# Performance work log

Hardware: AMD Instinct MI355X
Metric: run time of the kernel (lower is better)

The kernel has to match this reference:

```python
import jax, jax.numpy as jnp
import numpy as np

N, D, H, E, K = 16384, 1024, 4096, 8, 2
EPS = 1e-5


def setup_inputs() -> dict:
    key = jax.random.key(0)
    ks = jax.random.split(key, 12)
    s = 0.02
    return {
        "x": jax.random.normal(ks[0], (N, D), dtype=jnp.float32),
        "ln_g": jnp.ones((D,), jnp.float32),
        "ln_b": jnp.zeros((D,), jnp.float32),
        "r_w1": jax.random.normal(ks[1], (D, H // 2), jnp.float32) * s,
        "r_b1": jnp.zeros((H // 2,), jnp.float32),
        "r_w2": jax.random.normal(ks[2], (H // 2, E), jnp.float32) * s,
        "r_b2": jnp.zeros((E,), jnp.float32),
        "e_w1": jax.random.normal(ks[3], (E, D, H), jnp.float32) * s,
        "e_b1": jnp.zeros((E, H), jnp.float32),
        "e_w2": jax.random.normal(ks[4], (E, H, D), jnp.float32) * s,
        "e_b2": jnp.zeros((E, D), jnp.float32),
    }


def reference(x, ln_g, ln_b, r_w1, r_b1, r_w2, r_b2, e_w1, e_b1, e_w2, e_b2):
    # LayerNorm
    mu = jnp.mean(x, axis=-1, keepdims=True)
    var = jnp.mean(jnp.square(x - mu), axis=-1, keepdims=True)
    xn = (x - mu) * jax.lax.rsqrt(var + EPS) * ln_g + ln_b  # [N, D]

    # Router: Linear -> ReLU -> Linear -> softmax -> top-k, renormalize
    logits = jax.nn.relu(xn @ r_w1 + r_b1) @ r_w2 + r_b2  # [N, E]
    probs = jax.nn.softmax(logits, axis=-1)
    vals, idx = jax.lax.top_k(probs, K)  # [N, K]
    vals = vals / jnp.sum(vals, axis=-1, keepdims=True)

    # Dense expert dispatch: loop over fixed small E, weight by combine gate
    out = jnp.zeros_like(x)
    for e in range(E):
        gate = jnp.sum(vals * (idx == e).astype(vals.dtype), axis=-1)  # [N]
        h = jax.nn.relu(xn @ e_w1[e] + e_b1[e])  # dropout in eval mode -> identity
        y = h @ e_w2[e] + e_b2[e]  # [N, D]
        out = out + gate[:, None] * y
    return x + out
```

## Files before the change

kernel.cpp:

```cpp
#include <hip/hip_runtime.h>
#include <cstdint>
#include <cstddef>

typedef unsigned short u16;
typedef __attribute__((ext_vector_type(8))) short bf16x8;
typedef __attribute__((ext_vector_type(4))) float f32x4;

#define N_TOK 16384
#define DIM   1024
#define HID   4096
#define NEXP  8
#define HR    2048
#define TAU   0.02f
#define MAXMT 264

__device__ __forceinline__ u16 f2bf(float f) {
  union { float f; uint32_t u; } x; x.f = f;
  uint32_t r = x.u + 0x7FFFu + ((x.u >> 16) & 1u);
  return (u16)(r >> 16);
}
__device__ __forceinline__ float bf2f(u16 u) {
  union { uint32_t u; float f; } x; x.u = ((uint32_t)u) << 16; return x.f;
}

__device__ __forceinline__ void async16(const void* g, const void* l) {
  auto gp = reinterpret_cast<const __attribute__((address_space(1))) uint32_t*>(
      reinterpret_cast<uintptr_t>(g));
  auto lp = reinterpret_cast<__attribute__((address_space(3))) uint32_t*>(
      reinterpret_cast<uintptr_t>(l));
  __builtin_amdgcn_global_load_lds(gp, lp, 16, 0, 0);
}

__device__ __forceinline__ unsigned xcd_swz(unsigned flat, unsigned nwg) {
  const unsigned xcd = flat & 7u, lid = flat >> 3;
  const unsigned q = nwg >> 3, r = nwg & 7u;
  return (xcd < r ? xcd * (q + 1u) : r * (q + 1u) + (xcd - r) * q) + lid;
}

template<bool SPLIT>
__global__ __launch_bounds__(256)
void transpose_cvt(const float* __restrict__ src, u16* __restrict__ hi,
                   u16* __restrict__ lo, int R, int C)
{
  __shared__ float tile[32][33];
  const size_t bofs = (size_t)blockIdx.z * R * C;
  src += bofs; hi += bofs; if (SPLIT) lo += bofs;
  const int tx = threadIdx.x, ty = threadIdx.y;
  const int c0 = blockIdx.x * 32, r0 = blockIdx.y * 32;
#pragma unroll
  for (int i = 0; i < 4; ++i)
    tile[ty + i * 8][tx] = src[(size_t)(r0 + ty + i * 8) * C + c0 + tx];
  __syncthreads();
#pragma unroll
  for (int i = 0; i < 4; ++i) {
    float v = tile[tx][ty + i * 8];
    size_t o = (size_t)(c0 + ty + i * 8) * R + r0 + tx;
    u16 h = f2bf(v);
    hi[o] = h;
    if (SPLIT) lo[o] = f2bf(v - bf2f(h));
  }
}

__global__ __launch_bounds__(256)
void ln_kernel(const float* __restrict__ x, const float* __restrict__ g,
               const float* __restrict__ b, u16* __restrict__ xh,
               u16* __restrict__ xl, float* __restrict__ out)
{
  const int row = blockIdx.x;
  const int t = threadIdx.x;
  const float4 xv = ((const float4*)(x + (size_t)row * DIM))[t];
  float s = xv.x + xv.y + xv.z + xv.w;
  float q = xv.x * xv.x + xv.y * xv.y + xv.z * xv.z + xv.w * xv.w;
#pragma unroll
  for (int off = 32; off; off >>= 1) {
    s += __shfl_down(s, off, 64);
    q += __shfl_down(q, off, 64);
  }
  __shared__ float sm[8];
  __shared__ float mu_s, rs_s;
  const int lane = t & 63, wv = t >> 6;
  if (lane == 0) { sm[wv] = s; sm[wv + 4] = q; }
  __syncthreads();
  if (t == 0) {
    float S = sm[0] + sm[1] + sm[2] + sm[3];
    float Q = sm[4] + sm[5] + sm[6] + sm[7];
    float mu = S * (1.f / DIM);
    float var = Q * (1.f / DIM) - mu * mu;
    mu_s = mu; rs_s = rsqrtf(var + 1e-5f);
  }
  __syncthreads();
  const float mu = mu_s, rs = rs_s;
  const float4 gv = ((const float4*)g)[t];
  const float4 bv = ((const float4*)b)[t];
  float n0 = (xv.x - mu) * rs * gv.x + bv.x;
  float n1 = (xv.y - mu) * rs * gv.y + bv.y;
  float n2 = (xv.z - mu) * rs * gv.z + bv.z;
  float n3 = (xv.w - mu) * rs * gv.w + bv.w;
  ushort4 h, l;
  h.x = f2bf(n0); l.x = f2bf(n0 - bf2f(h.x));
  h.y = f2bf(n1); l.y = f2bf(n1 - bf2f(h.y));
  h.z = f2bf(n2); l.z = f2bf(n2 - bf2f(h.z));
  h.w = f2bf(n3); l.w = f2bf(n3 - bf2f(h.w));
  ((ushort4*)(xh + (size_t)row * DIM))[t] = h;
  ((ushort4*)(xl + (size_t)row * DIM))[t] = l;
  ((float4*)(out + (size_t)row * DIM))[t] = xv;
}

__global__ __launch_bounds__(256)
void logits_kernel(const u16* __restrict__ HrB, const float* __restrict__ w2,
                   float* __restrict__ logits)
{
  const int row = blockIdx.x, t = threadIdx.x;
  const u16* h = HrB + (size_t)row * HR;
  const ushort4* hv = (const ushort4*)(h + t * 8);
  ushort4 h0 = hv[0], h1 = hv[1];
  u16 hh[8] = {h0.x, h0.y, h0.z, h0.w, h1.x, h1.y, h1.z, h1.w};
  float p[8] = {0, 0, 0, 0, 0, 0, 0, 0};
#pragma unroll
  for (int j = 0; j < 8; ++j) {
    const int col = t * 8 + j;
    const float v = bf2f(hh[j]);
    const float4* wp = (const float4*)(w2 + (size_t)col * 8);
    float4 a = wp[0], b = wp[1];
    p[0] += v * a.x; p[1] += v * a.y; p[2] += v * a.z; p[3] += v * a.w;
    p[4] += v * b.x; p[5] += v * b.y; p[6] += v * b.z; p[7] += v * b.w;
  }
#pragma unroll
  for (int off = 32; off; off >>= 1)
#pragma unroll
    for (int e = 0; e < 8; ++e) p[e] += __shfl_down(p[e], off, 64);
  __shared__ float sm[4][8];
  const int lane = t & 63, wv = t >> 6;
  if (lane == 0) {
#pragma unroll
    for (int e = 0; e < 8; ++e) sm[wv][e] = p[e];
  }
  __syncthreads();
  if (t < 8)
    logits[(size_t)row * 8 + t] = sm[0][t] + sm[1][t] + sm[2][t] + sm[3][t];
}

__device__ __forceinline__ void load_logits(const float* logits, const float* b2,
                                            int row, float l[8]) {
  const float4* lp = (const float4*)(logits + (size_t)row * 8);
  float4 a = lp[0], b = lp[1];
  l[0] = a.x + b2[0]; l[1] = a.y + b2[1]; l[2] = a.z + b2[2]; l[3] = a.w + b2[3];
  l[4] = b.x + b2[4]; l[5] = b.y + b2[5]; l[6] = b.z + b2[6]; l[7] = b.w + b2[7];
}
__device__ __forceinline__ void top2(const float l[8], int& i0, float& l0,
                                     int& i1, float& l1) {
  i0 = 0; l0 = l[0];
#pragma unroll
  for (int e = 1; e < 8; ++e) if (l[e] > l0) { l0 = l[e]; i0 = e; }
  i1 = -1; l1 = -1e30f;
#pragma unroll
  for (int e = 0; e < 8; ++e) if (e != i0 && l[e] > l1) { l1 = l[e]; i1 = e; }
}

__global__ __launch_bounds__(256)
void pass_flag(float* __restrict__ logits, const float* __restrict__ b2,
               int* __restrict__ fixL, int* __restrict__ cntFix)
{
  __shared__ int lcnt;
  __shared__ int base;
  const int t = threadIdx.x;
  const int row = blockIdx.x * 256 + t;
  if (t == 0) lcnt = 0;
  float l[8]; load_logits(logits, b2, row, l);
  int i0, i1; float l0, l1;
  top2(l, i0, l0, i1, l1);
  float l2 = -1e30f;
#pragma unroll
  for (int e = 0; e < 8; ++e)
    if (e != i0 && e != i1 && l[e] > l2) l2 = l[e];
  const bool flag = (l1 - l2) < TAU;
  __syncthreads();
  int r = 0;
  if (flag) r = atomicAdd(&lcnt, 1);
  __syncthreads();
  if (t == 0) base = atomicAdd(cntFix, lcnt);
  __syncthreads();
  if (flag) {
    fixL[base + r] = row;
    float4 z = {0.f, 0.f, 0.f, 0.f};
    ((float4*)(logits + (size_t)row * 8))[0] = z;
    ((float4*)(logits + (size_t)row * 8))[1] = z;
  }
}

__global__ __launch_bounds__(256)
void pass_count(const float* __restrict__ logits, const float* __restrict__ b2,
                int* __restrict__ cnts)
{
  __shared__ int lcnt[NEXP];
  const int t = threadIdx.x;
  const int row = blockIdx.x * 256 + t;
  if (t < NEXP) lcnt[t] = 0;
  float l[8]; load_logits(logits, b2, row, l);
  int i0, i1; float l0, l1;
  top2(l, i0, l0, i1, l1);
  __syncthreads();
  atomicAdd(&lcnt[i0], 1);
  atomicAdd(&lcnt[i1], 1);
  __syncthreads();
  if (t < NEXP) atomicAdd(&cnts[t], lcnt[t]);
}

__global__ void scan_kernel(const int* __restrict__ cnts, int* __restrict__ offs,
                            int* __restrict__ tileOffs)
{
  if (threadIdx.x == 0) {
    int s = 0, ts = 0;
#pragma unroll
    for (int e = 0; e < NEXP; ++e) {
      offs[e] = s; s += cnts[e];
      tileOffs[e] = ts; ts += (cnts[e] + 127) >> 7;
    }
    offs[NEXP] = s;
    tileOffs[NEXP] = ts;
  }
}

__global__ __launch_bounds__(256)
void pass_scatter(const float* __restrict__ logits, const float* __restrict__ b2,
                  const int* __restrict__ offs, int* __restrict__ cnts2,
                  int* __restrict__ rowsC, float* __restrict__ gateC)
{
  __shared__ int lcnt[NEXP];
  __shared__ int sbase[NEXP];
  const int t = threadIdx.x;
  const int row = blockIdx.x * 256 + t;
  if (t < NEXP) lcnt[t] = 0;
  float l[8]; load_logits(logits, b2, row, l);
  int i0, i1; float l0, l1;
  top2(l, i0, l0, i1, l1);
  float tt = expf(l1 - l0);
  float g0 = 1.f / (1.f + tt);
  float g1 = tt / (1.f + tt);
  __syncthreads();
  int r0 = atomicAdd(&lcnt[i0], 1);
  int r1 = atomicAdd(&lcnt[i1], 1);
  __syncthreads();
  if (t < NEXP) sbase[t] = atomicAdd(&cnts2[t], lcnt[t]);
  __syncthreads();
  int p0 = offs[i0] + sbase[i0] + r0;
  int p1 = offs[i1] + sbase[i1] + r1;
  rowsC[p0] = row; gateC[p0] = g0;
  rowsC[p1] = row; gateC[p1] = g1;
}

template<int EPI, bool GATHER>
__global__ __launch_bounds__(512, 2)
void gemm_moe(const u16* __restrict__ A0, const u16* __restrict__ B0,
              int lda, int ldb, int K, int NT,
              size_t bStrideE, int biasStrideE,
              const int* __restrict__ counts,
              const int* __restrict__ offs, const int* __restrict__ tileOffs,
              const int* __restrict__ rowsC, const float* __restrict__ gatesC,
              const float* __restrict__ bias,
              u16* __restrict__ Cbf, float* __restrict__ Cf32, int ldc)
{
  const unsigned swz = xcd_swz(blockIdx.x, gridDim.x);
  const int mt = (int)(swz / (unsigned)NT);
  if (mt >= tileOffs[NEXP]) return;
  int e = 0;
#pragma unroll
  for (int i = 1; i < NEXP; ++i) if (tileOffs[i] <= mt) e = i;
  const int m0 = (mt - tileOffs[e]) * 128;
  const int n0 = (int)(swz % (unsigned)NT) * 256;
  const int Mq = counts[e];
  if (m0 >= Mq) return;

  const int off = offs[e];
  const int* rows = rowsC + off;
  const u16* B = B0 + (size_t)e * bStrideE;
  const float* bi = bias + (size_t)e * biasStrideE;

  __shared__ alignas(16) u16 As[8][128 * 32];
  __shared__ alignas(16) u16 Bs[4][256 * 32];

  const int t = threadIdx.x;
  const int numK = K >> 5;

  const int rloc = t >> 2;
  const int cb = ((t & 3) << 4) ^ (((t >> 5) & 1) << 5);
  const int csrc = cb >> 1;
  const int arow0 = m0 + rloc;
  const int amc = arow0 < Mq ? arow0 : (Mq - 1);
  const size_t agr = GATHER ? (size_t)rows[amc] : (size_t)(off + amc);
  const u16* aSrc = A0 + agr * lda + csrc;
  const u16* bSrc0 = B + (size_t)(n0 + rloc) * ldb + csrc;
  const u16* bSrc1 = B + (size_t)(n0 + 128 + rloc) * ldb + csrc;

#pragma unroll
  for (int h = 0; h < 6; ++h)
    async16(aSrc + h * 32, &As[h][t * 8]);
#pragma unroll
  for (int h = 0; h < 3; ++h) {
    async16(bSrc0 + h * 32, &Bs[h][t * 8]);
    async16(bSrc1 + h * 32, &Bs[h][4096 + t * 8]);
  }
  asm volatile("s_waitcnt vmcnt(4)" ::: "memory");
  __builtin_amdgcn_s_barrier();
  __builtin_amdgcn_sched_barrier(0);

  const int lane = t & 63, wv = t >> 6;
  const int wm = wv >> 2;
  const int wn = wv & 3;
  const int fr = lane & 15, fq = lane >> 4;

  int aIdx[4], bIdx[4];
#pragma unroll
  for (int mf = 0; mf < 4; ++mf) {
    const int r = wm * 64 + mf * 16 + fr;
    aIdx[mf] = r * 32 + ((fq * 8) ^ (((r >> 3) & 1) << 4));
  }
#pragma unroll
  for (int nf = 0; nf < 4; ++nf) {
    const int rb = wn * 64 + nf * 16 + fr;
    bIdx[nf] = rb * 32 + ((fq * 8) ^ (((rb >> 3) & 1) << 4));
  }

  f32x4 acc[4][4];
#pragma unroll
  for (int i = 0; i < 4; ++i)
#pragma unroll
    for (int j = 0; j < 4; ++j) acc[i][j] = (f32x4){0.f, 0.f, 0.f, 0.f};

  for (int T = 0; T < numK; ++T) {
    const u16* aLds = As[T & 7];
    const u16* bLds = Bs[T & 3];
    bf16x8 aF[4], bF[4];
#pragma unroll
    for (int i = 0; i < 4; ++i) {
      aF[i] = *(const bf16x8*)&aLds[aIdx[i]];
      bF[i] = *(const bf16x8*)&bLds[bIdx[i]];
    }
    if (T + 3 < numK) {
      async16(bSrc0 + (T + 3) * 32, &Bs[(T + 3) & 3][t * 8]);
      async16(bSrc1 + (T + 3) * 32, &Bs[(T + 3) & 3][4096 + t * 8]);
    }
    if (T + 6 < numK) async16(aSrc + (T + 6) * 32, &As[(T + 6) & 7][t * 8]);

    __builtin_amdgcn_s_setprio(1);
#pragma unroll
    for (int mf = 0; mf < 4; ++mf)
#pragma unroll
      for (int nf = 0; nf < 4; ++nf)
        acc[mf][nf] = __builtin_amdgcn_mfma_f32_16x16x32_bf16(
            aF[mf], bF[nf], acc[mf][nf], 0, 0, 0);
    __builtin_amdgcn_s_setprio(0);
    __builtin_amdgcn_sched_barrier(0);

    const int rem = numK - T;
    if (T == 0)        { asm volatile("s_waitcnt vmcnt(5)" ::: "memory"); }
    else if (T == 1)   { asm volatile("s_waitcnt vmcnt(6)" ::: "memory"); }
    else if (rem >= 7) { asm volatile("s_waitcnt vmcnt(7)" ::: "memory"); }
    else if (rem == 6) { asm volatile("s_waitcnt vmcnt(6)" ::: "memory"); }
    else if (rem == 5) { asm volatile("s_waitcnt vmcnt(5)" ::: "memory"); }
    else if (rem == 4) { asm volatile("s_waitcnt vmcnt(4)" ::: "memory"); }
    else if (rem == 3) { asm volatile("s_waitcnt vmcnt(2)" ::: "memory"); }
    else               { asm volatile("s_waitcnt vmcnt(0)" ::: "memory"); }
    __builtin_amdgcn_s_barrier();
    __builtin_amdgcn_sched_barrier(0);
  }

  float bv[4];
#pragma unroll
  for (int nf = 0; nf < 4; ++nf) bv[nf] = bi[n0 + wn * 64 + nf * 16 + fr];

#pragma unroll
  for (int mf = 0; mf < 4; ++mf)
#pragma unroll
    for (int r = 0; r < 4; ++r) {
      const int m = m0 + wm * 64 + mf * 16 + fq * 4 + r;
      if (m < Mq) {
        if constexpr (EPI == 2) {
          const size_t orow = (size_t)rows[m];
          const float g = gatesC[off + m];
#pragma unroll
          for (int nf = 0; nf < 4; ++nf) {
            const int n = n0 + wn * 64 + nf * 16 + fr;
            atomicAdd(&Cf32[orow * ldc + n], g * (acc[mf][nf][r] + bv[nf]));
          }
        } else {
#pragma unroll
          for (int nf = 0; nf < 4; ++nf) {
            const int n = n0 + wn * 64 + nf * 16 + fr;
            Cbf[(size_t)(off + m) * ldc + n] =
                f2bf(fmaxf(acc[mf][nf][r] + bv[nf], 0.f));
          }
        }
      }
    }
}

template<bool SPLIT, int EPI, bool GATHER>
__global__ __launch_bounds__(256, 2)
void gemm_bt(const u16* __restrict__ A0, const u16* __restrict__ A1,
             const u16* __restrict__ B0, const u16* __restrict__ B1,
             int lda, int ldb, int K, int M,
             const int* __restrict__ counts, int expertArg,
             const int* __restrict__ offs,
             const int* __restrict__ rowsC, const float* __restrict__ gatesC,
             const float* __restrict__ bias,
             const float* __restrict__ w2, float* __restrict__ logits,
             u16* __restrict__ Cbf, float* __restrict__ Cf32, int ldc)
{
  int expert, m0, n0;
  if (counts == nullptr) {
    const unsigned nwg = gridDim.x * gridDim.y;
    const unsigned flat = blockIdx.y * gridDim.x + blockIdx.x;
    const unsigned swz = xcd_swz(flat, nwg);
    expert = expertArg;
    m0 = (int)(swz / gridDim.x) * 128;
    n0 = (int)(swz % gridDim.x) * 128;
  } else {
    expert = expertArg;
    m0 = blockIdx.y * 128;
    n0 = blockIdx.x * 128;
  }

  const int Mq = counts ? counts[expert] : M;
  if (m0 >= Mq) return;
  const int off = offs ? offs[expert] : 0;
  const int* rows = rowsC ? rowsC + off : nullptr;
  const float* gates = gatesC ? gatesC + off : nullptr;
  const u16* B = B0;
  const u16* Bl = SPLIT ? B1 : nullptr;
  const float* bi = bias;
  const int z = (int)blockIdx.z;
  const int zOff = z * K;

  __shared__ u16 As0[128 * 32], Bs0[128 * 32];
  __shared__ u16 As1[SPLIT ? 128 * 32 : 8], Bs1[SPLIT ? 128 * 32 : 8];

  const int t = threadIdx.x;
  size_t aoff[2]; int acodd[2]; size_t boff[2];
#pragma unroll
  for (int i = 0; i < 2; ++i) {
    int gdx = i * 256 + t;
    int ar = gdx >> 2, ac = (gdx & 3) * 8;
    int am = m0 + ar;
    int amc = am < Mq ? am : (Mq - 1);
    int agr = GATHER ? rows[amc] : amc;
    aoff[i] = (size_t)agr * lda + ac + zOff;
    boff[i] = (size_t)(n0 + ar) * ldb + ac + zOff;
    acodd[i] = gdx * 8;
  }

  f32x4 acc[4][4];
#pragma unroll
  for (int i = 0; i < 4; ++i)
#pragma unroll
    for (int j = 0; j < 4; ++j) acc[i][j] = (f32x4){0.f, 0.f, 0.f, 0.f};

  const int lane = t & 63, wv = t >> 6;
  const int wm = (wv >> 1) * 64, wn = (wv & 1) * 64;
  const int fr = lane & 15, fq = lane >> 4;

  for (int k0 = 0; k0 < K; k0 += 32) {
    __syncthreads();
#pragma unroll
    for (int i = 0; i < 2; ++i) {
      async16(A0 + aoff[i] + k0, &As0[acodd[i]]);
      async16(B + boff[i] + k0, &Bs0[acodd[i]]);
      if (SPLIT) {
        async16(A1 + aoff[i] + k0, &As1[acodd[i]]);
        async16(Bl + boff[i] + k0, &Bs1[acodd[i]]);
      }
    }
    __syncthreads();
    bf16x8 af[4], bfr[4], af1[4], bf1[4];
#pragma unroll
    for (int xi = 0; xi < 4; ++xi) {
      af[xi]  = *(const bf16x8*)&As0[(wm + xi * 16 + fr) * 32 + fq * 8];
      bfr[xi] = *(const bf16x8*)&Bs0[(wn + xi * 16 + fr) * 32 + fq * 8];
      if (SPLIT) {
        af1[xi] = *(const bf16x8*)&As1[(wm + xi * 16 + fr) * 32 + fq * 8];
        bf1[xi] = *(const bf16x8*)&Bs1[(wn + xi * 16 + fr) * 32 + fq * 8];
      }
    }
#pragma unroll
    for (int mt = 0; mt < 4; ++mt)
#pragma unroll
      for (int nt = 0; nt < 4; ++nt) {
        acc[mt][nt] = __builtin_amdgcn_mfma_f32_16x16x32_bf16(af[mt], bfr[nt], acc[mt][nt], 0, 0, 0);
        if (SPLIT) {
          acc[mt][nt] = __builtin_amdgcn_mfma_f32_16x16x32_bf16(af[mt], bf1[nt], acc[mt][nt], 0, 0, 0);
          acc[mt][nt] = __builtin_amdgcn_mfma_f32_16x16x32_bf16(af1[mt], bfr[nt], acc[mt][nt], 0, 0, 0);
        }
      }
  }

  if constexpr (EPI == 3) {
    float w2v[4][8]; float b1v[4];
#pragma unroll
    for (int nt = 0; nt < 4; ++nt) {
      const int n = n0 + wn + nt * 16 + fr;
      b1v[nt] = bi[n];
      const float4* wp = (const float4*)(w2 + (size_t)n * 8);
      float4 wa = wp[0], wb = wp[1];
      w2v[nt][0] = wa.x; w2v[nt][1] = wa.y; w2v[nt][2] = wa.z; w2v[nt][3] = wa.w;
      w2v[nt][4] = wb.x; w2v[nt][5] = wb.y; w2v[nt][6] = wb.z; w2v[nt][7] = wb.w;
    }
#pragma unroll
    for (int mt = 0; mt < 4; ++mt) {
      float pe[4][8];
#pragma unroll
      for (int r = 0; r < 4; ++r)
#pragma unroll
        for (int ee = 0; ee < 8; ++ee) pe[r][ee] = 0.f;
#pragma unroll
      for (int nt = 0; nt < 4; ++nt)
#pragma unroll
        for (int r = 0; r < 4; ++r) {
          float v = fmaxf(acc[mt][nt][r] + b1v[nt], 0.f);
#pragma unroll
          for (int ee = 0; ee < 8; ++ee) pe[r][ee] += v * w2v[nt][ee];
        }
#pragma unroll
      for (int offx = 1; offx < 16; offx <<= 1)
#pragma unroll
        for (int r = 0; r < 4; ++r)
#pragma unroll
          for (int ee = 0; ee < 8; ++ee)
            pe[r][ee] += __shfl_xor(pe[r][ee], offx, 64);
      if (fr == 0) {
#pragma unroll
        for (int r = 0; r < 4; ++r) {
          const int m = m0 + wm + mt * 16 + fq * 4 + r;
          if (m < Mq) {
            const int lrow = GATHER ? rows[m] : m;
#pragma unroll
            for (int ee = 0; ee < 8; ++ee)
              atomicAdd(&logits[(size_t)lrow * 8 + ee], pe[r][ee]);
          }
        }
      }
    }
    return;
  }

#pragma unroll
  for (int mt = 0; mt < 4; ++mt) {
#pragma unroll
    for (int nt = 0; nt < 4; ++nt) {
      const int n = n0 + wn + nt * 16 + fr;
      const float bvv = (z == 0) ? bi[n] : 0.f;
#pragma unroll
      for (int r = 0; r < 4; ++r) {
        const int m = m0 + wm + mt * 16 + fq * 4 + r;
        if (m < Mq) {
          float v = acc[mt][nt][r] + bvv;
          if constexpr (EPI == 1) {
            Cbf[(size_t)m * ldc + n] = f2bf(fmaxf(v, 0.f));
          } else {
            atomicAdd(&Cf32[(size_t)rows[m] * ldc + n], gates[m] * v);
          }
        }
      }
    }
  }
}

extern "C" void kernel_launch(void* const* d_in, const int* in_sizes, int n_in,
                              void* d_out, int out_size, void* d_ws, size_t ws_size,
                              hipStream_t stream)
{
  const float* x    = (const float*)d_in[0];
  const float* ln_g = (const float*)d_in[1];
  const float* ln_b = (const float*)d_in[2];
  const float* r_w1 = (const float*)d_in[3];
  const float* r_b1 = (const float*)d_in[4];
  const float* r_w2 = (const float*)d_in[5];
  const float* r_b2 = (const float*)d_in[6];
  const float* e_w1 = (const float*)d_in[7];
  const float* e_b1 = (const float*)d_in[8];
  const float* e_w2 = (const float*)d_in[9];
  const float* e_b2 = (const float*)d_in[10];
  float* out = (float*)d_out;

  char* ws = (char*)d_ws;
  const size_t MB = 1024ull * 1024ull;
  u16*   xnhi = (u16*)(ws);
  u16*   xnlo = (u16*)(ws + 32 * MB);
  u16*   rw1h = (u16*)(ws + 64 * MB);
  u16*   rw1l = (u16*)(ws + 68 * MB);
  u16*   ew1t = (u16*)(ws + 72 * MB);
  u16*   ew2t = (u16*)(ws + 136 * MB);
  float* logits = (float*)(ws + 200 * MB);
  int*   rowsC  = (int*)(ws + 200 * MB + 512 * 1024);
  float* gateC  = (float*)(ws + 200 * MB + 640 * 1024);
  int*   fixL   = (int*)(ws + 200 * MB + 768 * 1024);
  int*   cntb   = (int*)(ws + 200 * MB + 832 * 1024);
  int*   cnts   = cntb;
  int*   cnts2  = cntb + 8;
  int*   offs   = cntb + 16;
  int*   cntFix = cntb + 25;
  int*   tileOffs = cntb + 32;
  u16*   Hbuf = (u16*)(ws + 201 * MB);
  u16*   HrB  = Hbuf;
  (void)in_sizes; (void)n_in; (void)out_size;

  const bool fused = ws_size >= 458ull * MB;

  hipMemsetAsync(cntb, 0, 256, stream);

  dim3 tb(32, 8);
  transpose_cvt<true ><<<dim3(HR / 32, DIM / 32, 1), tb, 0, stream>>>(r_w1, rw1h, rw1l, DIM, HR);
  transpose_cvt<false><<<dim3(HID / 32, DIM / 32, NEXP), tb, 0, stream>>>(e_w1, ew1t, nullptr, DIM, HID);
  transpose_cvt<false><<<dim3(DIM / 32, HID / 32, NEXP), tb, 0, stream>>>(e_w2, ew2t, nullptr, HID, DIM);

  ln_kernel<<<N_TOK, 256, 0, stream>>>(x, ln_g, ln_b, xnhi, xnlo, out);

  gemm_bt<false, 1, false><<<dim3(HR / 128, N_TOK / 128), 256, 0, stream>>>(
      xnhi, nullptr, rw1h, nullptr, DIM, DIM, DIM, N_TOK,
      nullptr, 0, nullptr, nullptr, nullptr, r_b1, nullptr, nullptr,
      HrB, nullptr, HR);

  logits_kernel<<<N_TOK, 256, 0, stream>>>(HrB, r_w2, logits);

  pass_flag<<<N_TOK / 256, 256, 0, stream>>>(logits, r_b2, fixL, cntFix);

  gemm_bt<true, 3, true><<<dim3(HR / 128, N_TOK / 128), 256, 0, stream>>>(
      xnhi, xnlo, rw1h, rw1l, DIM, DIM, DIM, N_TOK,
      cntFix, 0, nullptr, fixL, nullptr, r_b1, r_w2, logits,
      nullptr, nullptr, 0);

  pass_count<<<N_TOK / 256, 256, 0, stream>>>(logits, r_b2, cnts);
  scan_kernel<<<1, 64, 0, stream>>>(cnts, offs, tileOffs);
  pass_scatter<<<N_TOK / 256, 256, 0, stream>>>(logits, r_b2, offs, cnts2, rowsC, gateC);

  if (fused) {
    gemm_moe<1, true><<<dim3((HID / 256) * MAXMT), 512, 0, stream>>>(
        xnhi, ew1t, DIM, DIM, DIM, HID / 256,
        (size_t)HID * DIM, HID,
        cnts, offs, tileOffs, rowsC, nullptr, e_b1,
        Hbuf, nullptr, HID);
    gemm_moe<2, false><<<dim3((DIM / 256) * MAXMT), 512, 0, stream>>>(
        Hbuf, ew2t, HID, HID, HID, DIM / 256,
        (size_t)DIM * HID, DIM,
        cnts, offs, tileOffs, rowsC, gateC, e_b2,
        nullptr, out, DIM);
  } else {
    for (int e = 0; e < NEXP; ++e) {
      gemm_bt<false, 1, true><<<dim3(HID / 128, N_TOK / 128), 256, 0, stream>>>(
          xnhi, nullptr, ew1t + (size_t)e * HID * DIM, nullptr,
          DIM, DIM, DIM, N_TOK,
          cnts, e, offs, rowsC, nullptr, e_b1 + (size_t)e * HID, nullptr, nullptr,
          Hbuf, nullptr, HID);
      gemm_bt<false, 2, false><<<dim3(DIM / 128, N_TOK / 128, 2), 256, 0, stream>>>(
          Hbuf, nullptr, ew2t + (size_t)e * DIM * HID, nullptr,
          HID, HID, HID / 2, N_TOK,
          cnts, e, offs, rowsC, gateC, e_b2 + (size_t)e * DIM, nullptr, nullptr,
          nullptr, out, DIM);
    }
  }
}
```

Before: 1.582 ms.

## Double-buffer LDS fragment reads to overlap with MFMA in expert GEMM

```diff
diff --git a/kernel.cpp b/kernel.cpp
--- a/kernel.cpp
+++ b/kernel.cpp
@@ -292,18 +292,6 @@
   const u16* bSrc0 = B + (size_t)(n0 + rloc) * ldb + csrc;
   const u16* bSrc1 = B + (size_t)(n0 + 128 + rloc) * ldb + csrc;
 
-#pragma unroll
-  for (int h = 0; h < 6; ++h)
-    async16(aSrc + h * 32, &As[h][t * 8]);
-#pragma unroll
-  for (int h = 0; h < 3; ++h) {
-    async16(bSrc0 + h * 32, &Bs[h][t * 8]);
-    async16(bSrc1 + h * 32, &Bs[h][4096 + t * 8]);
-  }
-  asm volatile("s_waitcnt vmcnt(4)" ::: "memory");
-  __builtin_amdgcn_s_barrier();
-  __builtin_amdgcn_sched_barrier(0);
-
   const int lane = t & 63, wv = t >> 6;
   const int wm = wv >> 2;
   const int wn = wv & 3;
@@ -327,21 +315,23 @@
 #pragma unroll
     for (int j = 0; j < 4; ++j) acc[i][j] = (f32x4){0.f, 0.f, 0.f, 0.f};
 
-  for (int T = 0; T < numK; ++T) {
-    const u16* aLds = As[T & 7];
-    const u16* bLds = Bs[T & 3];
-    bf16x8 aF[4], bF[4];
+  auto stage = [&](int T) {
+    if (T + 3 < numK) {
+      async16(bSrc0 + (T + 3) * 32, &Bs[(T + 3) & 3][t * 8]);
+      async16(bSrc1 + (T + 3) * 32, &Bs[(T + 3) & 3][4096 + t * 8]);
+    }
+    if (T + 6 < numK) async16(aSrc + (T + 6) * 32, &As[(T + 6) & 7][t * 8]);
+  };
+  auto readFrags = [&](int tile, bf16x8* aF, bf16x8* bF) {
+    const u16* aLds = As[tile & 7];
+    const u16* bLds = Bs[tile & 3];
 #pragma unroll
     for (int i = 0; i < 4; ++i) {
       aF[i] = *(const bf16x8*)&aLds[aIdx[i]];
       bF[i] = *(const bf16x8*)&bLds[bIdx[i]];
     }
-    if (T + 3 < numK) {
-      async16(bSrc0 + (T + 3) * 32, &Bs[(T + 3) & 3][t * 8]);
-      async16(bSrc1 + (T + 3) * 32, &Bs[(T + 3) & 3][4096 + t * 8]);
-    }
-    if (T + 6 < numK) async16(aSrc + (T + 6) * 32, &As[(T + 6) & 7][t * 8]);
-
+  };
+  auto mfmaAll = [&](const bf16x8* aF, const bf16x8* bF) {
     __builtin_amdgcn_s_setprio(1);
 #pragma unroll
     for (int mf = 0; mf < 4; ++mf)
@@ -350,19 +340,43 @@
         acc[mf][nf] = __builtin_amdgcn_mfma_f32_16x16x32_bf16(
             aF[mf], bF[nf], acc[mf][nf], 0, 0, 0);
     __builtin_amdgcn_s_setprio(0);
+  };
+  auto endWait = [&](int T) {
     __builtin_amdgcn_sched_barrier(0);
-
     const int rem = numK - T;
-    if (T == 0)        { asm volatile("s_waitcnt vmcnt(5)" ::: "memory"); }
-    else if (T == 1)   { asm volatile("s_waitcnt vmcnt(6)" ::: "memory"); }
-    else if (rem >= 7) { asm volatile("s_waitcnt vmcnt(7)" ::: "memory"); }
-    else if (rem == 6) { asm volatile("s_waitcnt vmcnt(6)" ::: "memory"); }
-    else if (rem == 5) { asm volatile("s_waitcnt vmcnt(5)" ::: "memory"); }
-    else if (rem == 4) { asm volatile("s_waitcnt vmcnt(4)" ::: "memory"); }
-    else if (rem == 3) { asm volatile("s_waitcnt vmcnt(2)" ::: "memory"); }
+    if (T == 0)        { asm volatile("s_waitcnt vmcnt(3)" ::: "memory"); }
+    else if (rem >= 7) { asm volatile("s_waitcnt vmcnt(4)" ::: "memory"); }
+    else if (rem == 6) { asm volatile("s_waitcnt vmcnt(3)" ::: "memory"); }
+    else if (rem >= 4) { asm volatile("s_waitcnt vmcnt(2)" ::: "memory"); }
     else               { asm volatile("s_waitcnt vmcnt(0)" ::: "memory"); }
     __builtin_amdgcn_s_barrier();
     __builtin_amdgcn_sched_barrier(0);
+  };
+
+#pragma unroll
+  for (int h = 0; h < 6; ++h)
+    async16(aSrc + h * 32, &As[h][t * 8]);
+#pragma unroll
+  for (int h = 0; h < 3; ++h) {
+    async16(bSrc0 + h * 32, &Bs[h][t * 8]);
+    async16(bSrc1 + h * 32, &Bs[h][4096 + t * 8]);
+  }
+  asm volatile("s_waitcnt vmcnt(2)" ::: "memory");
+  __builtin_amdgcn_s_barrier();
+  __builtin_amdgcn_sched_barrier(0);
+
+  bf16x8 aC[4], bC[4], aN[4], bN[4];
+  readFrags(0, aC, bC);
+
+  for (int T = 0; T < numK; T += 2) {
+    stage(T);
+    if (T + 1 < numK) readFrags(T + 1, aN, bN);
+    mfmaAll(aC, bC);
+    endWait(T);
+    stage(T + 1);
+    if (T + 2 < numK) readFrags(T + 2, aC, bC);
+    mfmaAll(aN, bN);
+    endWait(T + 1);
   }
 
   float bv[4];
```

Measured after the change: 1.538 ms. 2.7% less time.

## Load expert B operand directly into registers and shrink MoE GEMM tile

Applied to the files above, without the earlier changes.

```diff
diff --git a/kernel.cpp b/kernel.cpp
--- a/kernel.cpp
+++ b/kernel.cpp
@@ -29,6 +29,13 @@
   auto lp = reinterpret_cast<__attribute__((address_space(3))) uint32_t*>(
       reinterpret_cast<uintptr_t>(l));
   __builtin_amdgcn_global_load_lds(gp, lp, 16, 0, 0);
+}
+
+__device__ __forceinline__ bf16x8 gload16(const u16* p) {
+  bf16x8 r;
+  asm volatile("global_load_dwordx4 %0, %1, off"
+               : "=&v"(r) : "v"(p) : "memory");
+  return r;
 }
 
 __device__ __forceinline__ unsigned xcd_swz(unsigned flat, unsigned nwg) {
@@ -250,7 +257,7 @@
 }
 
 template<int EPI, bool GATHER>
-__global__ __launch_bounds__(512, 2)
+__global__ __launch_bounds__(256, 4)
 void gemm_moe(const u16* __restrict__ A0, const u16* __restrict__ B0,
               int lda, int ldb, int K, int NT,
               size_t bStrideE, int biasStrideE,
@@ -267,7 +274,7 @@
 #pragma unroll
   for (int i = 1; i < NEXP; ++i) if (tileOffs[i] <= mt) e = i;
   const int m0 = (mt - tileOffs[e]) * 128;
-  const int n0 = (int)(swz % (unsigned)NT) * 256;
+  const int n0 = (int)(swz % (unsigned)NT) * 128;
   const int Mq = counts[e];
   if (m0 >= Mq) return;
 
@@ -276,93 +283,120 @@
   const u16* B = B0 + (size_t)e * bStrideE;
   const float* bi = bias + (size_t)e * biasStrideE;
 
-  __shared__ alignas(16) u16 As[8][128 * 32];
-  __shared__ alignas(16) u16 Bs[4][256 * 32];
+  __shared__ alignas(16) u16 As[4][128 * 32];
 
   const int t = threadIdx.x;
   const int numK = K >> 5;
 
-  const int rloc = t >> 2;
-  const int cb = ((t & 3) << 4) ^ (((t >> 5) & 1) << 5);
-  const int csrc = cb >> 1;
-  const int arow0 = m0 + rloc;
-  const int amc = arow0 < Mq ? arow0 : (Mq - 1);
-  const size_t agr = GATHER ? (size_t)rows[amc] : (size_t)(off + amc);
-  const u16* aSrc = A0 + agr * lda + csrc;
-  const u16* bSrc0 = B + (size_t)(n0 + rloc) * ldb + csrc;
-  const u16* bSrc1 = B + (size_t)(n0 + 128 + rloc) * ldb + csrc;
-
-#pragma unroll
-  for (int h = 0; h < 6; ++h)
-    async16(aSrc + h * 32, &As[h][t * 8]);
+  const u16* aptr[2]; int adst[2];
+#pragma unroll
+  for (int i = 0; i < 2; ++i) {
+    const int gdx = i * 256 + t;
+    const int ar = gdx >> 2;
+    const int cb = ((gdx & 3) << 4) ^ (((gdx >> 5) & 1) << 5);
+    const int am = m0 + ar;
+    const int amc = am < Mq ? am : (Mq - 1);
+    const size_t agr = GATHER ? (size_t)rows[amc] : (size_t)(off + amc);
+    aptr[i] = A0 + agr * lda + (cb >> 1);
+    adst[i] = gdx * 8;
+  }
+
+  const int lane = t & 63, wv = t >> 6;
+  const int wm = wv >> 1;
+  const int wn = wv & 1;
+  const int fr = lane & 15, fq = lane >> 4;
+
+  int aIdx[4];
+#pragma unroll
+  for (int mf = 0; mf < 4; ++mf) {
+    const int r = wm * 64 + mf * 16 + fr;
+    aIdx[mf] = r * 32 + ((fq * 8) ^ (((r >> 3) & 1) << 4));
+  }
+  const u16* bp[4];
+#pragma unroll
+  for (int nf = 0; nf < 4; ++nf)
+    bp[nf] = B + (size_t)(n0 + wn * 64 + nf * 16 + fr) * ldb + fq * 8;
+
+  f32x4 acc[4][4];
+#pragma unroll
+  for (int i = 0; i < 4; ++i)
+#pragma unroll
+    for (int j = 0; j < 4; ++j) acc[i][j] = (f32x4){0.f, 0.f, 0.f, 0.f};
+
+  bf16x8 b0[4], b1[4];
+
 #pragma unroll
   for (int h = 0; h < 3; ++h) {
-    async16(bSrc0 + h * 32, &Bs[h][t * 8]);
-    async16(bSrc1 + h * 32, &Bs[h][4096 + t * 8]);
-  }
+    async16(aptr[0] + h * 32, &As[h][adst[0]]);
+    async16(aptr[1] + h * 32, &As[h][adst[1]]);
+  }
+#pragma unroll
+  for (int nf = 0; nf < 4; ++nf) b0[nf] = gload16(bp[nf]);
+#pragma unroll
+  for (int nf = 0; nf < 4; ++nf) b1[nf] = gload16(bp[nf] + 32);
   asm volatile("s_waitcnt vmcnt(4)" ::: "memory");
   __builtin_amdgcn_s_barrier();
   __builtin_amdgcn_sched_barrier(0);
 
-  const int lane = t & 63, wv = t >> 6;
-  const int wm = wv >> 2;
-  const int wn = wv & 3;
-  const int fr = lane & 15, fq = lane >> 4;
-
-  int aIdx[4], bIdx[4];
-#pragma unroll
-  for (int mf = 0; mf < 4; ++mf) {
-    const int r = wm * 64 + mf * 16 + fr;
-    aIdx[mf] = r * 32 + ((fq * 8) ^ (((r >> 3) & 1) << 4));
-  }
-#pragma unroll
-  for (int nf = 0; nf < 4; ++nf) {
-    const int rb = wn * 64 + nf * 16 + fr;
-    bIdx[nf] = rb * 32 + ((fq * 8) ^ (((rb >> 3) & 1) << 4));
-  }
-
-  f32x4 acc[4][4];
-#pragma unroll
-  for (int i = 0; i < 4; ++i)
-#pragma unroll
-    for (int j = 0; j < 4; ++j) acc[i][j] = (f32x4){0.f, 0.f, 0.f, 0.f};
-
-  for (int T = 0; T < numK; ++T) {
-    const u16* aLds = As[T & 7];
-    const u16* bLds = Bs[T & 3];
-    bf16x8 aF[4], bF[4];
-#pragma unroll
-    for (int i = 0; i < 4; ++i) {
-      aF[i] = *(const bf16x8*)&aLds[aIdx[i]];
-      bF[i] = *(const bf16x8*)&bLds[bIdx[i]];
-    }
+  auto phase = [&](int T, bf16x8 (&bs)[4]) {
     if (T + 3 < numK) {
-      async16(bSrc0 + (T + 3) * 32, &Bs[(T + 3) & 3][t * 8]);
-      async16(bSrc1 + (T + 3) * 32, &Bs[(T + 3) & 3][4096 + t * 8]);
-    }
-    if (T + 6 < numK) async16(aSrc + (T + 6) * 32, &As[(T + 6) & 7][t * 8]);
-
+      async16(aptr[0] + (size_t)(T + 3) * 32, &As[(T + 3) & 3][adst[0]]);
+      async16(aptr[1] + (size_t)(T + 3) * 32, &As[(T + 3) & 3][adst[1]]);
+    }
+    const u16* aL = As[T & 3];
+    bf16x8 aF[4];
+#pragma unroll
+    for (int mf = 0; mf < 4; ++mf) aF[mf] = *(const bf16x8*)&aL[aIdx[mf]];
     __builtin_amdgcn_s_setprio(1);
 #pragma unroll
     for (int mf = 0; mf < 4; ++mf)
 #pragma unroll
       for (int nf = 0; nf < 4; ++nf)
         acc[mf][nf] = __builtin_amdgcn_mfma_f32_16x16x32_bf16(
-            aF[mf], bF[nf], acc[mf][nf], 0, 0, 0);
+            aF[mf], bs[nf], acc[mf][nf], 0, 0, 0);
     __builtin_amdgcn_s_setprio(0);
+    if (T + 2 < numK) {
+#pragma unroll
+      for (int nf = 0; nf < 4; ++nf)
+        bs[nf] = gload16(bp[nf] + (size_t)(T + 2) * 32);
+    }
     __builtin_amdgcn_sched_barrier(0);
-
-    const int rem = numK - T;
-    if (T == 0)        { asm volatile("s_waitcnt vmcnt(5)" ::: "memory"); }
-    else if (T == 1)   { asm volatile("s_waitcnt vmcnt(6)" ::: "memory"); }
-    else if (rem >= 7) { asm volatile("s_waitcnt vmcnt(7)" ::: "memory"); }
-    else if (rem == 6) { asm volatile("s_waitcnt vmcnt(6)" ::: "memory"); }
-    else if (rem == 5) { asm volatile("s_waitcnt vmcnt(5)" ::: "memory"); }
-    else if (rem == 4) { asm volatile("s_waitcnt vmcnt(4)" ::: "memory"); }
-    else if (rem == 3) { asm volatile("s_waitcnt vmcnt(2)" ::: "memory"); }
-    else               { asm volatile("s_waitcnt vmcnt(0)" ::: "memory"); }
+    if (numK - T >= 4) { asm volatile("s_waitcnt vmcnt(6)" ::: "memory"); }
+    else               { asm volatile("s_waitcnt vmcnt(4)" ::: "memory"); }
     __builtin_amdgcn_s_barrier();
     __builtin_amdgcn_sched_barrier(0);
+  };
+
+  for (int T = 0; T + 2 < numK; T += 2) {
+    phase(T, b0);
+    phase(T + 1, b1);
+  }
+
+  {
+    const u16* aL = As[(numK - 2) & 3];
+    bf16x8 aF[4];
+#pragma unroll
+    for (int mf = 0; mf < 4; ++mf) aF[mf] = *(const bf16x8*)&aL[aIdx[mf]];
+#pragma unroll
+    for (int mf = 0; mf < 4; ++mf)
+#pragma unroll
+      for (int nf = 0; nf < 4; ++nf)
+        acc[mf][nf] = __builtin_amdgcn_mfma_f32_16x16x32_bf16(
+            aF[mf], b0[nf], acc[mf][nf], 0, 0, 0);
+  }
+  asm volatile("s_waitcnt vmcnt(0)" ::: "memory");
+  __builtin_amdgcn_sched_barrier(0);
+  {
+    const u16* aL = As[(numK - 1) & 3];
+    bf16x8 aF[4];
+#pragma unroll
+    for (int mf = 0; mf < 4; ++mf) aF[mf] = *(const bf16x8*)&aL[aIdx[mf]];
+#pragma unroll
+    for (int mf = 0; mf < 4; ++mf)
+#pragma unroll
+      for (int nf = 0; nf < 4; ++nf)
+        acc[mf][nf] = __builtin_amdgcn_mfma_f32_16x16x32_bf16(
+            aF[mf], b1[nf], acc[mf][nf], 0, 0, 0);
   }
 
   float bv[4];
@@ -633,13 +667,13 @@
   pass_scatter<<<N_TOK / 256, 256, 0, stream>>>(logits, r_b2, offs, cnts2, rowsC, gateC);
 
   if (fused) {
-    gemm_moe<1, true><<<dim3((HID / 256) * MAXMT), 512, 0, stream>>>(
-        xnhi, ew1t, DIM, DIM, DIM, HID / 256,
+    gemm_moe<1, true><<<dim3((HID / 128) * MAXMT), 256, 0, stream>>>(
+        xnhi, ew1t, DIM, DIM, DIM, HID / 128,
         (size_t)HID * DIM, HID,
         cnts, offs, tileOffs, rowsC, nullptr, e_b1,
         Hbuf, nullptr, HID);
-    gemm_moe<2, false><<<dim3((DIM / 256) * MAXMT), 512, 0, stream>>>(
-        Hbuf, ew2t, HID, HID, HID, DIM / 256,
+    gemm_moe<2, false><<<dim3((DIM / 128) * MAXMT), 256, 0, stream>>>(
+        Hbuf, ew2t, HID, HID, HID, DIM / 128,
         (size_t)DIM * HID, DIM,
         cnts, offs, tileOffs, rowsC, gateC, e_b2,
         nullptr, out, DIM);
```

Result: slower. 2.247 ms (+42.1%).
